# Kernel optimization log

Hardware: AMD Instinct MI355X
Metric: run time of the kernel (lower is better)

The kernel has to match this reference:

```python
import jax, jax.numpy as jnp
import numpy as np

D = 1024
LEAF_DIM = 512
DEPTH = 3
NUM_LEAVES = 2 ** DEPTH          # 8
NUM_NODES = NUM_LEAVES - 1       # 7
B, T = 4, 2048


def setup_inputs() -> dict:
    key = jax.random.key(0)
    ks = jax.random.split(key, 9)
    sD = 1.0 / np.sqrt(D)
    sH = 1.0 / np.sqrt(LEAF_DIM)
    return {
        "x": jax.random.normal(ks[0], (B, T, D), dtype=jnp.float32),
        "node_kernel": jax.random.normal(ks[1], (D, NUM_NODES), dtype=jnp.float32) * sD,
        "node_bias": jnp.zeros((NUM_NODES,), dtype=jnp.float32),
        "w1a": jax.random.normal(ks[2], (NUM_LEAVES, D, LEAF_DIM), dtype=jnp.float32) * sD,
        "w1b": jax.random.normal(ks[3], (NUM_LEAVES, D, LEAF_DIM), dtype=jnp.float32) * sD,
        "b1a": jnp.zeros((NUM_LEAVES, LEAF_DIM), dtype=jnp.float32),
        "b1b": jnp.zeros((NUM_LEAVES, LEAF_DIM), dtype=jnp.float32),
        "w2": jax.random.normal(ks[4], (NUM_LEAVES, LEAF_DIM, D), dtype=jnp.float32) * sH,
        "b2": jnp.zeros((NUM_LEAVES, D), dtype=jnp.float32),
    }


def reference(x, node_kernel, node_bias, w1a, w1b, b1a, b1b, w2, b2):
    Bx, Tx, Dx = x.shape
    L = NUM_LEAVES
    # hierarchical sigmoid gates over tree nodes: (B,T,num_nodes)
    c = jax.nn.sigmoid(jnp.einsum("btd,dn->btn", x, node_kernel) + node_bias)
    # interleave [c_i, 1-c_i] -> (B,T,2*num_nodes,1), matching original stack+reshape
    c_nc = jnp.stack([c, 1.0 - c], axis=-1).reshape(Bx, Tx, -1)[..., None]
    # build per-leaf mixture weights by descending the tree (depth is a small constant)
    mixture = jnp.ones((Bx, Tx, L), dtype=x.dtype)
    for d in range(DEPTH):
        n2 = 2 ** (d + 1)  # 2 * n_nodes at this level
        mixture = mixture.reshape(Bx, Tx, n2, L // n2) * c_nc[..., :n2, :]
    mixture = mixture.reshape(Bx, Tx, L)
    # per-leaf GLU MLP, batched over the leaf axis
    h = (jnp.einsum("btd,ldh->btlh", x, w1a) + b1a) * (
        jnp.einsum("btd,ldh->btlh", x, w1b) + b1b
    )  # (B,T,L,leaf_dim)
    y = jnp.einsum("btlh,lhd->btld", h, w2) + b2  # (B,T,L,D)
    # weighted combine over leaves
    return (y * mixture[..., None]).sum(axis=-2)  # (B,T,D)
```

## Files before the change

kernel.cpp:

```cpp
#include <hip/hip_runtime.h>


typedef unsigned short u16;
typedef __attribute__((ext_vector_type(8))) short bf16x8;
typedef __attribute__((ext_vector_type(8))) unsigned short u16x8;
typedef __attribute__((ext_vector_type(4))) float f32x4;

__device__ __forceinline__ u16 f2bf(float f) {
  unsigned int u = __builtin_bit_cast(unsigned int, f);
  u += 0x7FFFu + ((u >> 16) & 1u);
  return (u16)(u >> 16);
}

__device__ __forceinline__ void gload16(const void* g, void* l) {
  __builtin_amdgcn_global_load_lds(
      (const __attribute__((address_space(1))) unsigned int*)g,
      (__attribute__((address_space(3))) unsigned int*)l, 16, 0, 0);
}

__device__ __forceinline__ f32x4 MFMA(bf16x8 a, bf16x8 b, f32x4 c) {
  return __builtin_amdgcn_mfma_f32_16x16x32_bf16(a, b, c, 0, 0, 0);
}

#define BARX()                              \
  do {                                      \
    __builtin_amdgcn_sched_barrier(0);      \
    __builtin_amdgcn_s_barrier();           \
    __builtin_amdgcn_sched_barrier(0);      \
  } while (0)

#define VMC(n)                                             \
  do {                                                     \
    __builtin_amdgcn_sched_barrier(0);                     \
    asm volatile("s_waitcnt vmcnt(" #n ")" ::: "memory");  \
    __builtin_amdgcn_sched_barrier(0);                     \
  } while (0)

__global__ void k_gatecast(const float* __restrict__ x, const float* __restrict__ nk,
                           const float* __restrict__ nb, float* __restrict__ mix,
                           u16* __restrict__ xb) {
  int token = blockIdx.x * 4 + (threadIdx.x >> 6);
  int lane = threadIdx.x & 63;
  const float* xr = x + (size_t)token * 1024;
  u16* xbr = xb + (size_t)token * 1024;
  float a0 = 0.f, a1 = 0.f, a2 = 0.f, a3 = 0.f;
#pragma unroll
  for (int j = 0; j < 2; ++j) {
    int base = j * 512 + lane * 8;
    float4 p0 = *(const float4*)&xr[base];
    float4 p1 = *(const float4*)&xr[base + 4];
    float v[8] = {p0.x, p0.y, p0.z, p0.w, p1.x, p1.y, p1.z, p1.w};
    u16x8 o;
#pragma unroll
    for (int t = 0; t < 8; ++t) {
      const float* nkd = nk + (size_t)(base + t) * 7;
      a0 = fmaf(v[t], nkd[0], a0);
      a1 = fmaf(v[t], nkd[1], a1);
      a2 = fmaf(v[t], nkd[2], a2);
      a3 = fmaf(v[t], nkd[3], a3);
      o[t] = f2bf(v[t]);
    }
    *(u16x8*)&xbr[base] = o;
  }
#pragma unroll
  for (int off = 32; off >= 1; off >>= 1) {
    a0 += __shfl_xor(a0, off);
    a1 += __shfl_xor(a1, off);
    a2 += __shfl_xor(a2, off);
    a3 += __shfl_xor(a3, off);
  }
  if (lane == 0) {
    float v4[4] = {a0 + nb[0], a1 + nb[1], a2 + nb[2], a3 + nb[3]};
    float cn[8];
#pragma unroll
    for (int i = 0; i < 4; ++i) {
      float s = 1.f / (1.f + expf(-v4[i]));
      cn[2 * i] = s;
      cn[2 * i + 1] = 1.f - s;
    }
    float* mr = mix + (size_t)token * 8;
#pragma unroll
    for (int l = 0; l < 8; ++l) mr[l] = cn[l >> 2] * cn[l >> 1] * cn[l];
  }
}

__global__ void k_transpose_cast(const float* __restrict__ in, u16* __restrict__ out,
                                 int R, int C, long out_rstride, long leaf_base) {
  __shared__ float tile[32][33];
  int l = blockIdx.z;
  int c0 = blockIdx.x * 32, r0 = blockIdx.y * 32;
  const float* inl = in + (size_t)l * R * C;
  int tc = threadIdx.x & 31, tr = threadIdx.x >> 5;
#pragma unroll
  for (int i = 0; i < 4; ++i) {
    int r = tr + i * 8;
    tile[r][tc] = inl[(size_t)(r0 + r) * C + c0 + tc];
  }
  __syncthreads();
  u16* outl = out + (size_t)l * leaf_base;
#pragma unroll
  for (int i = 0; i < 4; ++i) {
    int c = tr + i * 8;
    outl[(size_t)(c0 + c) * out_rstride + r0 + tc] = f2bf(tile[tc][c]);
  }
}

__global__ void k_transpose_w1(const float* __restrict__ w1a, const float* __restrict__ w1b,
                               u16* __restrict__ WaT, u16* __restrict__ WbT) {
  __shared__ float tile[32][33];
  int z = blockIdx.z;
  int l = z & 7;
  const float* in = (z < 8) ? w1a : w1b;
  u16* out = (z < 8) ? WaT : WbT;
  int c0 = blockIdx.x * 32, r0 = blockIdx.y * 32;
  const float* inl = in + (size_t)l * 1024 * 512;
  int tc = threadIdx.x & 31, tr = threadIdx.x >> 5;
#pragma unroll
  for (int i = 0; i < 4; ++i) {
    int r = tr + i * 8;
    tile[r][tc] = inl[(size_t)(r0 + r) * 512 + c0 + tc];
  }
  __syncthreads();
  u16* outl = out + (size_t)l * 512 * 1024;
#pragma unroll
  for (int i = 0; i < 4; ++i) {
    int c = tr + i * 8;
    outl[(size_t)(c0 + c) * 1024 + r0 + tc] = f2bf(tile[tc][c]);
  }
}

__global__ __launch_bounds__(256, 2) void k_glu_gemm(
    const u16* __restrict__ Xb, const u16* __restrict__ Wa, const u16* __restrict__ Wb,
    const float* __restrict__ b1a, const float* __restrict__ b1b,
    const float* __restrict__ mix, u16* __restrict__ H) {
  constexpr int K = 1024, NT = 32;
  __shared__ alignas(16) u16 smem[24576];
  const int tid = threadIdx.x;
  const int logical = (blockIdx.x & 7) * 256 + (blockIdx.x >> 3);
  const int xcd_chunk = logical >> 8;
  const int i_ = logical & 255;
  const int bn = xcd_chunk * 4 + (i_ & 3);
  const int bm = i_ >> 2;
  const int m0 = bm * 128, n0 = bn * 128;
  const int wid = tid >> 6, lane = tid & 63;
  const int wm = (wid >> 1) * 64, wn = (wid & 1) * 64;
  const int fr = lane & 15, fk = lane >> 4;

  const int c0_ = tid, c1_ = tid + 256;
  const int r0_ = c0_ >> 2, s0_ = ((c0_ & 3) ^ ((r0_ >> 1) & 3)) * 8;
  const int r1_ = c1_ >> 2, s1_ = ((c1_ & 3) ^ ((r1_ >> 1) & 3)) * 8;

#define STG1(v)                                                                     \
  do {                                                                              \
    const int kb = (v) * 32;                                                        \
    u16* dA = smem + ((v) & 1) * 4096;                                              \
    u16* dBa = smem + 8192 + ((v) & 1) * 4096;                                      \
    u16* dBb = smem + 16384 + ((v) & 1) * 4096;                                     \
    gload16(&Xb[(size_t)(m0 + r0_) * K + kb + s0_], &dA[c0_ * 8]);                  \
    gload16(&Xb[(size_t)(m0 + r1_) * K + kb + s1_], &dA[c1_ * 8]);                  \
    gload16(&Wa[(size_t)(n0 + r0_) * K + kb + s0_], &dBa[c0_ * 8]);                 \
    gload16(&Wa[(size_t)(n0 + r1_) * K + kb + s1_], &dBa[c1_ * 8]);                 \
    gload16(&Wb[(size_t)(n0 + r0_) * K + kb + s0_], &dBb[c0_ * 8]);                 \
    gload16(&Wb[(size_t)(n0 + r1_) * K + kb + s1_], &dBb[c1_ * 8]);                 \
  } while (0)

  f32x4 accA[4][4], accB[4][4];
#pragma unroll
  for (int i = 0; i < 4; ++i)
#pragma unroll
    for (int j = 0; j < 4; ++j) {
      accA[i][j] = (f32x4)0.0f;
      accB[i][j] = (f32x4)0.0f;
    }

  const int slot_ = (fk ^ ((fr >> 1) & 3)) * 8;

  STG1(0);
  VMC(0);
  BARX();
  for (int u = 0; u < NT; ++u) {
    if (u + 1 < NT) STG1(u + 1);
    __builtin_amdgcn_sched_barrier(0);
    const u16* A_ = smem + (u & 1) * 4096;
    const u16* Ba_ = smem + 8192 + (u & 1) * 4096;
    const u16* Bb_ = smem + 16384 + (u & 1) * 4096;
    bf16x8 a_[4], ba_[4], bb_[4];
#pragma unroll
    for (int i = 0; i < 4; ++i) {
      a_[i]  = *(const bf16x8*)&A_[(wm + i * 16 + fr) * 32 + slot_];
      ba_[i] = *(const bf16x8*)&Ba_[(wn + i * 16 + fr) * 32 + slot_];
      bb_[i] = *(const bf16x8*)&Bb_[(wn + i * 16 + fr) * 32 + slot_];
    }
    __builtin_amdgcn_s_setprio(1);
#pragma unroll
    for (int i = 0; i < 4; ++i)
#pragma unroll
      for (int j = 0; j < 4; ++j) {
        accA[i][j] = MFMA(a_[i], ba_[j], accA[i][j]);
        accB[i][j] = MFMA(a_[i], bb_[j], accB[i][j]);
      }
    __builtin_amdgcn_s_setprio(0);
    VMC(0);
    BARX();
  }
#undef STG1

  const int leaf = n0 >> 9;
  const float* b1al = b1a + (leaf << 9);
  const float* b1bl = b1b + (leaf << 9);
  u16* hs = smem;
#pragma unroll
  for (int mf = 0; mf < 4; ++mf)
#pragma unroll
    for (int r = 0; r < 4; ++r) {
      int row_l = wm + mf * 16 + fk * 4 + r;
      float mv = mix[(size_t)(m0 + row_l) * 8 + leaf];
#pragma unroll
      for (int nf = 0; nf < 4; ++nf) {
        int col_l = wn + nf * 16 + fr;
        int hc = (n0 + col_l) & 511;
        float va = accA[mf][nf][r] + b1al[hc];
        float vb = accB[mf][nf][r] + b1bl[hc];
        hs[row_l * 128 + col_l] = f2bf(va * vb * mv);
      }
    }
  BARX();
#pragma unroll
  for (int j = 0; j < 8; ++j) {
    int idx = j * 256 + tid;
    int row_l = idx >> 4;
    int cc = (idx & 15) * 8;
    *(u16x8*)&H[(size_t)(m0 + row_l) * 4096 + n0 + cc] =
        *(const u16x8*)&hs[row_l * 128 + cc];
  }
}

__global__ __launch_bounds__(256, 4) void k_gemm2s(
    const u16* __restrict__ Hm, const u16* __restrict__ W2T,
    const float* __restrict__ b2, const float* __restrict__ mix,
    float* __restrict__ out, float* __restrict__ P1) {
  constexpr int K = 4096, KH = 2048, NT = KH / 32;
  __shared__ alignas(16) u16 smem[16384];
  const int tid = threadIdx.x;
  const int logical = (blockIdx.x & 7) * 128 + (blockIdx.x >> 3);
  const int xcd_chunk = logical >> 7;
  const int i_ = logical & 127;
  const int kc = i_ >> 6;
  const int bn = i_ & 7;
  const int bm = xcd_chunk * 8 + ((i_ >> 3) & 7);
  const int m0 = bm * 128, n0 = bn * 128;
  const size_t kbase = (size_t)kc * KH;
  const int wid = tid >> 6, lane = tid & 63;
  const int wm = (wid >> 1) * 64, wn = (wid & 1) * 64;
  const int fr = lane & 15, fk = lane >> 4;

  const int c0_ = tid, c1_ = tid + 256;
  const int r0_ = c0_ >> 2, s0_ = ((c0_ & 3) ^ ((r0_ >> 1) & 3)) * 8;
  const int r1_ = c1_ >> 2, s1_ = ((c1_ & 3) ^ ((r1_ >> 1) & 3)) * 8;

#define STG2(v)                                                                       \
  do {                                                                                \
    const int kb = (v) * 32;                                                          \
    u16* dA = smem + ((v) & 1) * 4096;                                                \
    u16* dB = smem + 8192 + ((v) & 1) * 4096;                                         \
    gload16(&Hm[(size_t)(m0 + r0_) * K + kbase + kb + s0_], &dA[c0_ * 8]);            \
    gload16(&Hm[(size_t)(m0 + r1_) * K + kbase + kb + s1_], &dA[c1_ * 8]);            \
    gload16(&W2T[(size_t)(n0 + r0_) * K + kbase + kb + s0_], &dB[c0_ * 8]);           \
    gload16(&W2T[(size_t)(n0 + r1_) * K + kbase + kb + s1_], &dB[c1_ * 8]);           \
  } while (0)

  f32x4 acc[4][4];
#pragma unroll
  for (int i = 0; i < 4; ++i)
#pragma unroll
    for (int j = 0; j < 4; ++j) acc[i][j] = (f32x4)0.0f;

  const int slot_ = (fk ^ ((fr >> 1) & 3)) * 8;

  STG2(0);
  VMC(0);
  BARX();
  for (int u = 0; u < NT; ++u) {
    if (u + 1 < NT) STG2(u + 1);
    __builtin_amdgcn_sched_barrier(0);
    const u16* A_ = smem + (u & 1) * 4096;
    const u16* B_ = smem + 8192 + (u & 1) * 4096;
    bf16x8 a_[4], b_[4];
#pragma unroll
    for (int i = 0; i < 4; ++i) {
      a_[i] = *(const bf16x8*)&A_[(wm + i * 16 + fr) * 32 + slot_];
      b_[i] = *(const bf16x8*)&B_[(wn + i * 16 + fr) * 32 + slot_];
    }
    __builtin_amdgcn_s_setprio(1);
#pragma unroll
    for (int i = 0; i < 4; ++i)
#pragma unroll
      for (int j = 0; j < 4; ++j)
        acc[i][j] = MFMA(a_[i], b_[j], acc[i][j]);
    __builtin_amdgcn_s_setprio(0);
    VMC(0);
    BARX();
  }
#undef STG2

  float* dst = (kc == 0) ? out : P1;
  float* os = (float*)smem;
  const int myhalf = wid >> 1;
#pragma unroll
  for (int half = 0; half < 2; ++half) {
    BARX();
    if (myhalf == half) {
#pragma unroll
      for (int nf = 0; nf < 4; ++nf) {
        int col_l = wn + nf * 16 + fr;
        float bc[8];
        if (kc == 0) {
#pragma unroll
          for (int l = 0; l < 8; ++l) bc[l] = b2[l * 1024 + n0 + col_l];
        }
#pragma unroll
        for (int mf = 0; mf < 4; ++mf)
#pragma unroll
          for (int r = 0; r < 4; ++r) {
            int row_lh = mf * 16 + fk * 4 + r;
            float v = acc[mf][nf][r];
            if (kc == 0) {
              const float* mr = mix + (size_t)(m0 + half * 64 + row_lh) * 8;
              float bias = 0.f;
#pragma unroll
              for (int l = 0; l < 8; ++l) bias = fmaf(mr[l], bc[l], bias);
              v += bias;
            }
            os[row_lh * 128 + col_l] = v;
          }
      }
    }
    BARX();
#pragma unroll
    for (int j = 0; j < 8; ++j) {
      int idx = j * 256 + tid;
      int row_lh = idx >> 5;
      int cc = (idx & 31) * 4;
      *(float4*)&dst[(size_t)(m0 + half * 64 + row_lh) * 1024 + n0 + cc] =
          *(const float4*)&os[row_lh * 128 + cc];
    }
  }
}

__global__ void k_add(float* __restrict__ out, const float* __restrict__ P1) {
  size_t i = (size_t)blockIdx.x * 256 + threadIdx.x;
  float4 a = ((const float4*)out)[i];
  float4 b = ((const float4*)P1)[i];
  a.x += b.x; a.y += b.y; a.z += b.z; a.w += b.w;
  ((float4*)out)[i] = a;
}

extern "C" void kernel_launch(void* const* d_in, const int* in_sizes, int n_in,
                              void* d_out, int out_size, void* d_ws, size_t ws_size,
                              hipStream_t stream) {
  const float* x   = (const float*)d_in[0];
  const float* nk  = (const float*)d_in[1];
  const float* nb  = (const float*)d_in[2];
  const float* w1a = (const float*)d_in[3];
  const float* w1b = (const float*)d_in[4];
  const float* b1a = (const float*)d_in[5];
  const float* b1b = (const float*)d_in[6];
  const float* w2  = (const float*)d_in[7];
  const float* b2  = (const float*)d_in[8];
  float* out = (float*)d_out;

  char* ws = (char*)d_ws;
  float* mix = (float*)ws;
  u16* Xb  = (u16*)(ws + 262144);
  u16* WaT = (u16*)(ws + 262144 + 16777216);
  u16* WbT = (u16*)(ws + 262144 + 16777216 + 8388608);
  u16* W2T = (u16*)(ws + 262144 + 16777216 + 2 * 8388608);
  u16* Hs  = (u16*)(ws + 262144 + 16777216 + 3 * 8388608);
  float* P1 = (float*)(ws + 262144);

  k_gatecast<<<2048, 256, 0, stream>>>(x, nk, nb, mix, Xb);
  k_transpose_w1<<<dim3(16, 32, 16), 256, 0, stream>>>(w1a, w1b, WaT, WbT);
  k_transpose_cast<<<dim3(32, 16, 8), 256, 0, stream>>>(w2, W2T, 512, 1024, 4096L, 512L);
  k_glu_gemm<<<2048, 256, 0, stream>>>(Xb, WaT, WbT, b1a, b1b, mix, Hs);
  k_gemm2s<<<1024, 256, 0, stream>>>(Hs, W2T, b2, mix, out, P1);
  k_add<<<8192, 256, 0, stream>>>(out, P1);
}
```

Before: 275.7 us.

## Restructure GLU GEMM into 8-wave blocks with BK=64 staggered per-operand pipeline

Rewrites the first GLU GEMM kernel to use 512 threads (8 waves, each owning a 64x32 sub-tile) with a K-step of 64 instead of 32, halving the number of main-loop iterations. Global-to-LDS loads for A, Wa and Wb are split into three separately issued stages that are interleaved with the MFMA phases, with partial vmcnt waits, so memory traffic overlaps compute. The LDS swizzle is changed to an 8-way XOR to match the wider rows. LDS use grows to 96 KB per block and occupancy is limited to one block per CU, which trades latency hiding from multiple blocks for deeper intra-block pipelining.

New measurement: 346.8 us. 25.8% more time.

```diff
diff --git a/kernel.cpp b/kernel.cpp
--- a/kernel.cpp
+++ b/kernel.cpp
@@ -129,12 +129,14 @@
   }
 }
 
-__global__ __launch_bounds__(256, 2) void k_glu_gemm(
+__global__ __launch_bounds__(512, 1) void k_glu_gemm(
     const u16* __restrict__ Xb, const u16* __restrict__ Wa, const u16* __restrict__ Wb,
     const float* __restrict__ b1a, const float* __restrict__ b1b,
     const float* __restrict__ mix, u16* __restrict__ H) {
-  constexpr int K = 1024, NT = 32;
-  __shared__ alignas(16) u16 smem[24576];
+  constexpr int K = 1024, NT = 16;
+  __shared__ alignas(16) u16 sA[2][8192];
+  __shared__ alignas(16) u16 sBa[2][8192];
+  __shared__ alignas(16) u16 sBb[2][8192];
   const int tid = threadIdx.x;
   const int logical = (blockIdx.x & 7) * 256 + (blockIdx.x >> 3);
   const int xcd_chunk = logical >> 8;
@@ -143,72 +145,147 @@
   const int bm = i_ >> 2;
   const int m0 = bm * 128, n0 = bn * 128;
   const int wid = tid >> 6, lane = tid & 63;
-  const int wm = (wid >> 1) * 64, wn = (wid & 1) * 64;
+  const int wm = (wid >> 2) * 64, wn = (wid & 3) * 32;
   const int fr = lane & 15, fk = lane >> 4;
 
-  const int c0_ = tid, c1_ = tid + 256;
-  const int r0_ = c0_ >> 2, s0_ = ((c0_ & 3) ^ ((r0_ >> 1) & 3)) * 8;
-  const int r1_ = c1_ >> 2, s1_ = ((c1_ & 3) ^ ((r1_ >> 1) & 3)) * 8;
-
-#define STG1(v)                                                                     \
-  do {                                                                              \
-    const int kb = (v) * 32;                                                        \
-    u16* dA = smem + ((v) & 1) * 4096;                                              \
-    u16* dBa = smem + 8192 + ((v) & 1) * 4096;                                      \
-    u16* dBb = smem + 16384 + ((v) & 1) * 4096;                                     \
-    gload16(&Xb[(size_t)(m0 + r0_) * K + kb + s0_], &dA[c0_ * 8]);                  \
-    gload16(&Xb[(size_t)(m0 + r1_) * K + kb + s1_], &dA[c1_ * 8]);                  \
-    gload16(&Wa[(size_t)(n0 + r0_) * K + kb + s0_], &dBa[c0_ * 8]);                 \
-    gload16(&Wa[(size_t)(n0 + r1_) * K + kb + s1_], &dBa[c1_ * 8]);                 \
-    gload16(&Wb[(size_t)(n0 + r0_) * K + kb + s0_], &dBb[c0_ * 8]);                 \
-    gload16(&Wb[(size_t)(n0 + r1_) * K + kb + s1_], &dBb[c1_ * 8]);                 \
-  } while (0)
-
-  f32x4 accA[4][4], accB[4][4];
+  const int ca = tid, cb = tid + 512;
+  const int ra_ = ca >> 3, sa_ = ((ca & 7) ^ (ra_ & 7)) * 8;
+  const int rb_ = cb >> 3, sb_ = ((cb & 7) ^ (rb_ & 7)) * 8;
+
+#define STG_A(v)                                                              \
+  do {                                                                       \
+    const int kb = (v) * 64;                                                 \
+    gload16(&Xb[(size_t)(m0 + ra_) * K + kb + sa_], &sA[(v) & 1][ca * 8]);   \
+    gload16(&Xb[(size_t)(m0 + rb_) * K + kb + sb_], &sA[(v) & 1][cb * 8]);   \
+  } while (0)
+#define STG_BA(v)                                                             \
+  do {                                                                       \
+    const int kb = (v) * 64;                                                 \
+    gload16(&Wa[(size_t)(n0 + ra_) * K + kb + sa_], &sBa[(v) & 1][ca * 8]);  \
+    gload16(&Wa[(size_t)(n0 + rb_) * K + kb + sb_], &sBa[(v) & 1][cb * 8]);  \
+  } while (0)
+#define STG_BB(v)                                                             \
+  do {                                                                       \
+    const int kb = (v) * 64;                                                 \
+    gload16(&Wb[(size_t)(n0 + ra_) * K + kb + sa_], &sBb[(v) & 1][ca * 8]);  \
+    gload16(&Wb[(size_t)(n0 + rb_) * K + kb + sb_], &sBb[(v) & 1][cb * 8]);  \
+  } while (0)
+
+  f32x4 accA[4][2], accB[4][2];
 #pragma unroll
   for (int i = 0; i < 4; ++i)
 #pragma unroll
-    for (int j = 0; j < 4; ++j) {
+    for (int j = 0; j < 2; ++j) {
       accA[i][j] = (f32x4)0.0f;
       accB[i][j] = (f32x4)0.0f;
     }
 
-  const int slot_ = (fk ^ ((fr >> 1) & 3)) * 8;
-
-  STG1(0);
-  VMC(0);
+  const int sw0 = ((fk) ^ (fr & 7)) * 8;
+  const int sw1 = ((4 + fk) ^ (fr & 7)) * 8;
+
+  STG_A(0); STG_BA(0); STG_BB(0);
+
+  bf16x8 aA[4], ba_[2], bb_[2];
+  for (int u = 0; u < NT - 1; ++u) {
+    const u16* A_ = sA[u & 1];
+    const u16* Ba_ = sBa[u & 1];
+    const u16* Bb_ = sBb[u & 1];
+    VMC(2);
+    BARX();
+    STG_A(u + 1);
+    __builtin_amdgcn_sched_barrier(0);
+#pragma unroll
+    for (int m = 0; m < 4; ++m) aA[m] = *(const bf16x8*)&A_[(wm + m * 16 + fr) * 64 + sw0];
+#pragma unroll
+    for (int n = 0; n < 2; ++n) ba_[n] = *(const bf16x8*)&Ba_[(wn + n * 16 + fr) * 64 + sw0];
+    __builtin_amdgcn_s_setprio(1);
+#pragma unroll
+    for (int m = 0; m < 4; ++m)
+#pragma unroll
+      for (int n = 0; n < 2; ++n) accA[m][n] = MFMA(aA[m], ba_[n], accA[m][n]);
+    __builtin_amdgcn_s_setprio(0);
+    VMC(2);
+    BARX();
+    STG_BA(u + 1);
+    __builtin_amdgcn_sched_barrier(0);
+#pragma unroll
+    for (int n = 0; n < 2; ++n) bb_[n] = *(const bf16x8*)&Bb_[(wn + n * 16 + fr) * 64 + sw0];
+    __builtin_amdgcn_s_setprio(1);
+#pragma unroll
+    for (int m = 0; m < 4; ++m)
+#pragma unroll
+      for (int n = 0; n < 2; ++n) accB[m][n] = MFMA(aA[m], bb_[n], accB[m][n]);
+    __builtin_amdgcn_s_setprio(0);
+    BARX();
+    STG_BB(u + 1);
+    __builtin_amdgcn_sched_barrier(0);
+#pragma unroll
+    for (int m = 0; m < 4; ++m) aA[m] = *(const bf16x8*)&A_[(wm + m * 16 + fr) * 64 + sw1];
+#pragma unroll
+    for (int n = 0; n < 2; ++n) ba_[n] = *(const bf16x8*)&Ba_[(wn + n * 16 + fr) * 64 + sw1];
+    __builtin_amdgcn_s_setprio(1);
+#pragma unroll
+    for (int m = 0; m < 4; ++m)
+#pragma unroll
+      for (int n = 0; n < 2; ++n) accA[m][n] = MFMA(aA[m], ba_[n], accA[m][n]);
+    __builtin_amdgcn_s_setprio(0);
+    BARX();
+#pragma unroll
+    for (int n = 0; n < 2; ++n) bb_[n] = *(const bf16x8*)&Bb_[(wn + n * 16 + fr) * 64 + sw1];
+    __builtin_amdgcn_s_setprio(1);
+#pragma unroll
+    for (int m = 0; m < 4; ++m)
+#pragma unroll
+      for (int n = 0; n < 2; ++n) accB[m][n] = MFMA(aA[m], bb_[n], accB[m][n]);
+    __builtin_amdgcn_s_setprio(0);
+  }
+  {
+    const int u = NT - 1;
+    const u16* A_ = sA[u & 1];
+    const u16* Ba_ = sBa[u & 1];
+    const u16* Bb_ = sBb[u & 1];
+    VMC(2);
+    BARX();
+#pragma unroll
+    for (int m = 0; m < 4; ++m) aA[m] = *(const bf16x8*)&A_[(wm + m * 16 + fr) * 64 + sw0];
+#pragma unroll
+    for (int n = 0; n < 2; ++n) ba_[n] = *(const bf16x8*)&Ba_[(wn + n * 16 + fr) * 64 + sw0];
+#pragma unroll
+    for (int m = 0; m < 4; ++m)
+#pragma unroll
+      for (int n = 0; n < 2; ++n) accA[m][n] = MFMA(aA[m], ba_[n], accA[m][n]);
+    VMC(0);
+    BARX();
+#pragma unroll
+    for (int n = 0; n < 2; ++n) bb_[n] = *(const bf16x8*)&Bb_[(wn + n * 16 + fr) * 64 + sw0];
+#pragma unroll
+    for (int m = 0; m < 4; ++m)
+#pragma unroll
+      for (int n = 0; n < 2; ++n) accB[m][n] = MFMA(aA[m], bb_[n], accB[m][n]);
+#pragma unroll
+    for (int m = 0; m < 4; ++m) aA[m] = *(const bf16x8*)&A_[(wm + m * 16 + fr) * 64 + sw1];
+#pragma unroll
+    for (int n = 0; n < 2; ++n) ba_[n] = *(const bf16x8*)&Ba_[(wn + n * 16 + fr) * 64 + sw1];
+#pragma unroll
+    for (int m = 0; m < 4; ++m)
+#pragma unroll
+      for (int n = 0; n < 2; ++n) accA[m][n] = MFMA(aA[m], ba_[n], accA[m][n]);
+#pragma unroll
+    for (int n = 0; n < 2; ++n) bb_[n] = *(const bf16x8*)&Bb_[(wn + n * 16 + fr) * 64 + sw1];
+#pragma unroll
+    for (int m = 0; m < 4; ++m)
+#pragma unroll
+      for (int n = 0; n < 2; ++n) accB[m][n] = MFMA(aA[m], bb_[n], accB[m][n]);
+  }
+#undef STG_A
+#undef STG_BA
+#undef STG_BB
+
   BARX();
-  for (int u = 0; u < NT; ++u) {
-    if (u + 1 < NT) STG1(u + 1);
-    __builtin_amdgcn_sched_barrier(0);
-    const u16* A_ = smem + (u & 1) * 4096;
-    const u16* Ba_ = smem + 8192 + (u & 1) * 4096;
-    const u16* Bb_ = smem + 16384 + (u & 1) * 4096;
-    bf16x8 a_[4], ba_[4], bb_[4];
-#pragma unroll
-    for (int i = 0; i < 4; ++i) {
-      a_[i]  = *(const bf16x8*)&A_[(wm + i * 16 + fr) * 32 + slot_];
-      ba_[i] = *(const bf16x8*)&Ba_[(wn + i * 16 + fr) * 32 + slot_];
-      bb_[i] = *(const bf16x8*)&Bb_[(wn + i * 16 + fr) * 32 + slot_];
-    }
-    __builtin_amdgcn_s_setprio(1);
-#pragma unroll
-    for (int i = 0; i < 4; ++i)
-#pragma unroll
-      for (int j = 0; j < 4; ++j) {
-        accA[i][j] = MFMA(a_[i], ba_[j], accA[i][j]);
-        accB[i][j] = MFMA(a_[i], bb_[j], accB[i][j]);
-      }
-    __builtin_amdgcn_s_setprio(0);
-    VMC(0);
-    BARX();
-  }
-#undef STG1
-
   const int leaf = n0 >> 9;
   const float* b1al = b1a + (leaf << 9);
   const float* b1bl = b1b + (leaf << 9);
-  u16* hs = smem;
+  u16* hs = &sA[0][0];
 #pragma unroll
   for (int mf = 0; mf < 4; ++mf)
 #pragma unroll
@@ -216,7 +293,7 @@
       int row_l = wm + mf * 16 + fk * 4 + r;
       float mv = mix[(size_t)(m0 + row_l) * 8 + leaf];
 #pragma unroll
-      for (int nf = 0; nf < 4; ++nf) {
+      for (int nf = 0; nf < 2; ++nf) {
         int col_l = wn + nf * 16 + fr;
         int hc = (n0 + col_l) & 511;
         float va = accA[mf][nf][r] + b1al[hc];
@@ -226,8 +303,8 @@
     }
   BARX();
 #pragma unroll
-  for (int j = 0; j < 8; ++j) {
-    int idx = j * 256 + tid;
+  for (int j = 0; j < 4; ++j) {
+    int idx = j * 512 + tid;
     int row_l = idx >> 4;
     int cc = (idx & 15) * 8;
     *(u16x8*)&H[(size_t)(m0 + row_l) * 4096 + n0 + cc] =
@@ -381,7 +458,7 @@
   k_gatecast<<<2048, 256, 0, stream>>>(x, nk, nb, mix, Xb);
   k_transpose_w1<<<dim3(16, 32, 16), 256, 0, stream>>>(w1a, w1b, WaT, WbT);
   k_transpose_cast<<<dim3(32, 16, 8), 256, 0, stream>>>(w2, W2T, 512, 1024, 4096L, 512L);
-  k_glu_gemm<<<2048, 256, 0, stream>>>(Xb, WaT, WbT, b1a, b1b, mix, Hs);
+  k_glu_gemm<<<2048, 512, 0, stream>>>(Xb, WaT, WbT, b1a, b1b, mix, Hs);
   k_gemm2s<<<1024, 256, 0, stream>>>(Hs, W2T, b2, mix, out, P1);
   k_add<<<8192, 256, 0, stream>>>(out, P1);
 }
```

## Prefetch A tiles two stages ahead and use one barrier per k-step

Applied to the files above, without the earlier changes.

In both GEMM kernels the activation (A) tile is now triple-buffered and loaded two k-steps ahead, while the weight tiles stay double-buffered one step ahead. The wait and barrier move to the top of each iteration, using a partial vmcnt wait so the newest A load can stay in flight. This removes one of the two barriers per iteration and gives global loads more time to overlap with MFMA work. The cost is more LDS per block: 56 KB for the GLU kernel and 40 KB for the second GEMM, which at 4 blocks per CU uses the full LDS and could limit occupancy.

After: 274.4 us. No clear change (-0.4%).

```diff
diff --git a/kernel.cpp b/kernel.cpp
--- a/kernel.cpp
+++ b/kernel.cpp
@@ -134,7 +134,7 @@
     const float* __restrict__ b1a, const float* __restrict__ b1b,
     const float* __restrict__ mix, u16* __restrict__ H) {
   constexpr int K = 1024, NT = 32;
-  __shared__ alignas(16) u16 smem[24576];
+  __shared__ alignas(16) u16 smem[28672];
   const int tid = threadIdx.x;
   const int logical = (blockIdx.x & 7) * 256 + (blockIdx.x >> 3);
   const int xcd_chunk = logical >> 8;
@@ -150,16 +150,24 @@
   const int r0_ = c0_ >> 2, s0_ = ((c0_ & 3) ^ ((r0_ >> 1) & 3)) * 8;
   const int r1_ = c1_ >> 2, s1_ = ((c1_ & 3) ^ ((r1_ >> 1) & 3)) * 8;
 
-#define STG1(v)                                                                     \
+#define STG_A(v)                                                                    \
   do {                                                                              \
     const int kb = (v) * 32;                                                        \
-    u16* dA = smem + ((v) & 1) * 4096;                                              \
-    u16* dBa = smem + 8192 + ((v) & 1) * 4096;                                      \
-    u16* dBb = smem + 16384 + ((v) & 1) * 4096;                                     \
+    u16* dA = smem + ((v) % 3) * 4096;                                              \
     gload16(&Xb[(size_t)(m0 + r0_) * K + kb + s0_], &dA[c0_ * 8]);                  \
     gload16(&Xb[(size_t)(m0 + r1_) * K + kb + s1_], &dA[c1_ * 8]);                  \
+  } while (0)
+#define STG_BA(v)                                                                   \
+  do {                                                                              \
+    const int kb = (v) * 32;                                                        \
+    u16* dBa = smem + 12288 + ((v) & 1) * 4096;                                     \
     gload16(&Wa[(size_t)(n0 + r0_) * K + kb + s0_], &dBa[c0_ * 8]);                 \
     gload16(&Wa[(size_t)(n0 + r1_) * K + kb + s1_], &dBa[c1_ * 8]);                 \
+  } while (0)
+#define STG_BB(v)                                                                   \
+  do {                                                                              \
+    const int kb = (v) * 32;                                                        \
+    u16* dBb = smem + 20480 + ((v) & 1) * 4096;                                     \
     gload16(&Wb[(size_t)(n0 + r0_) * K + kb + s0_], &dBb[c0_ * 8]);                 \
     gload16(&Wb[(size_t)(n0 + r1_) * K + kb + s1_], &dBb[c1_ * 8]);                 \
   } while (0)
@@ -175,15 +183,17 @@
 
   const int slot_ = (fk ^ ((fr >> 1) & 3)) * 8;
 
-  STG1(0);
-  VMC(0);
-  BARX();
+  STG_BA(0); STG_BB(0); STG_A(0); STG_A(1);
+
   for (int u = 0; u < NT; ++u) {
-    if (u + 1 < NT) STG1(u + 1);
+    if (u + 1 < NT) { VMC(2); } else { VMC(0); }
+    BARX();
+    if (u + 1 < NT) { STG_BA(u + 1); STG_BB(u + 1); }
+    if (u + 2 < NT) STG_A(u + 2);
     __builtin_amdgcn_sched_barrier(0);
-    const u16* A_ = smem + (u & 1) * 4096;
-    const u16* Ba_ = smem + 8192 + (u & 1) * 4096;
-    const u16* Bb_ = smem + 16384 + (u & 1) * 4096;
+    const u16* A_  = smem + (u % 3) * 4096;
+    const u16* Ba_ = smem + 12288 + (u & 1) * 4096;
+    const u16* Bb_ = smem + 20480 + (u & 1) * 4096;
     bf16x8 a_[4], ba_[4], bb_[4];
 #pragma unroll
     for (int i = 0; i < 4; ++i) {
@@ -200,11 +210,12 @@
         accB[i][j] = MFMA(a_[i], bb_[j], accB[i][j]);
       }
     __builtin_amdgcn_s_setprio(0);
-    VMC(0);
-    BARX();
-  }
-#undef STG1
-
+  }
+#undef STG_A
+#undef STG_BA
+#undef STG_BB
+
+  BARX();
   const int leaf = n0 >> 9;
   const float* b1al = b1a + (leaf << 9);
   const float* b1bl = b1b + (leaf << 9);
@@ -240,7 +251,7 @@
     const float* __restrict__ b2, const float* __restrict__ mix,
     float* __restrict__ out, float* __restrict__ P1) {
   constexpr int K = 4096, KH = 2048, NT = KH / 32;
-  __shared__ alignas(16) u16 smem[16384];
+  __shared__ alignas(16) u16 smem[20480];
   const int tid = threadIdx.x;
   const int logical = (blockIdx.x & 7) * 128 + (blockIdx.x >> 3);
   const int xcd_chunk = logical >> 7;
@@ -258,13 +269,17 @@
   const int r0_ = c0_ >> 2, s0_ = ((c0_ & 3) ^ ((r0_ >> 1) & 3)) * 8;
   const int r1_ = c1_ >> 2, s1_ = ((c1_ & 3) ^ ((r1_ >> 1) & 3)) * 8;
 
-#define STG2(v)                                                                       \
+#define STG2_A(v)                                                                     \
   do {                                                                                \
     const int kb = (v) * 32;                                                          \
-    u16* dA = smem + ((v) & 1) * 4096;                                                \
-    u16* dB = smem + 8192 + ((v) & 1) * 4096;                                         \
+    u16* dA = smem + ((v) % 3) * 4096;                                                \
     gload16(&Hm[(size_t)(m0 + r0_) * K + kbase + kb + s0_], &dA[c0_ * 8]);            \
     gload16(&Hm[(size_t)(m0 + r1_) * K + kbase + kb + s1_], &dA[c1_ * 8]);            \
+  } while (0)
+#define STG2_B(v)                                                                     \
+  do {                                                                                \
+    const int kb = (v) * 32;                                                          \
+    u16* dB = smem + 12288 + ((v) & 1) * 4096;                                        \
     gload16(&W2T[(size_t)(n0 + r0_) * K + kbase + kb + s0_], &dB[c0_ * 8]);           \
     gload16(&W2T[(size_t)(n0 + r1_) * K + kbase + kb + s1_], &dB[c1_ * 8]);           \
   } while (0)
@@ -277,14 +292,16 @@
 
   const int slot_ = (fk ^ ((fr >> 1) & 3)) * 8;
 
-  STG2(0);
-  VMC(0);
-  BARX();
+  STG2_B(0); STG2_A(0); STG2_A(1);
+
   for (int u = 0; u < NT; ++u) {
-    if (u + 1 < NT) STG2(u + 1);
+    if (u + 1 < NT) { VMC(2); } else { VMC(0); }
+    BARX();
+    if (u + 1 < NT) STG2_B(u + 1);
+    if (u + 2 < NT) STG2_A(u + 2);
     __builtin_amdgcn_sched_barrier(0);
-    const u16* A_ = smem + (u & 1) * 4096;
-    const u16* B_ = smem + 8192 + (u & 1) * 4096;
+    const u16* A_ = smem + (u % 3) * 4096;
+    const u16* B_ = smem + 12288 + (u & 1) * 4096;
     bf16x8 a_[4], b_[4];
 #pragma unroll
     for (int i = 0; i < 4; ++i) {
@@ -298,10 +315,9 @@
       for (int j = 0; j < 4; ++j)
         acc[i][j] = MFMA(a_[i], b_[j], acc[i][j]);
     __builtin_amdgcn_s_setprio(0);
-    VMC(0);
-    BARX();
-  }
-#undef STG2
+  }
+#undef STG2_A
+#undef STG2_B
 
   float* dst = (kc == 0) ? out : P1;
   float* os = (float*)smem;
```
